# Performance work log

Hardware: AMD Instinct MI355X
Metric: run time of the kernel (lower is better)

## Reference

```python
import jax, jax.numpy as jnp
import numpy as np

N = 12000   # num_node
D = 128     # hiddenSize
HID = 256   # hidden_channels
B = 512     # batch
L = 20      # citing history length
F = 400     # title_vec + journal_vec
FF = 512    # transformer dim_feedforward
NH = 4      # heads
STDV = float(1.0 / np.sqrt(D))


def _unif(k, shape):
    return jax.random.uniform(k, shape, jnp.float32, -STDV, STDV)


def setup_inputs():
    key = jax.random.key(0)
    ks = jax.random.split(key, 40)
    inp = {}
    inp['embedding'] = _unif(ks[0], (N, D))
    inp['f1_w'] = _unif(ks[1], (D, F)); inp['f1_b'] = _unif(ks[2], (D,))
    # two GNN modules, each a 2-layer GCN (assumed structure)
    inp['gcn0_w1'] = _unif(ks[3], (D, HID)); inp['gcn0_b1'] = _unif(ks[4], (HID,))
    inp['gcn0_w2'] = _unif(ks[5], (HID, D)); inp['gcn0_b2'] = _unif(ks[6], (D,))
    inp['gcn1_w1'] = _unif(ks[7], (D, HID)); inp['gcn1_b1'] = _unif(ks[8], (HID,))
    inp['gcn1_w2'] = _unif(ks[9], (HID, D)); inp['gcn1_b2'] = _unif(ks[10], (D,))
    # transformer encoder layer (post-norm, relu), reset_parameters makes ALL weights uniform
    inp['in_proj_w'] = _unif(ks[11], (3 * D, D)); inp['in_proj_b'] = _unif(ks[12], (3 * D,))
    inp['out_proj_w'] = _unif(ks[13], (D, D)); inp['out_proj_b'] = _unif(ks[14], (D,))
    inp['ln1_s'] = _unif(ks[15], (D,)); inp['ln1_b'] = _unif(ks[16], (D,))
    inp['ff1_w'] = _unif(ks[17], (FF, D)); inp['ff1_b'] = _unif(ks[18], (FF,))
    inp['ff2_w'] = _unif(ks[19], (D, FF)); inp['ff2_b'] = _unif(ks[20], (D,))
    inp['ln2_s'] = _unif(ks[21], (D,)); inp['ln2_b'] = _unif(ks[22], (D,))
    # forward inputs
    inp['adj_mat'] = jax.random.uniform(ks[23], (N, N), jnp.float32) * (2.0 / N)  # ~row-stochastic
    inp['node_feature'] = jax.random.normal(ks[24], (N, F), jnp.float32)
    inp['H_content'] = jax.random.normal(ks[25], (B, 10), jnp.float32)  # unused in forward
    inp['citing'] = jax.random.randint(ks[26], (B,), 0, N)
    inp['h_items'] = jax.random.randint(ks[27], (B,), 0, N)  # unused in forward
    inp['u_seqs'] = jax.random.randint(ks[28], (B, L), 0, N)
    inp['u_seqs_num'] = jax.random.randint(ks[29], (B,), 1, L)  # unused in forward
    return inp


def _layer_norm(x, s, b):
    m = x.mean(-1, keepdims=True)
    v = ((x - m) ** 2).mean(-1, keepdims=True)
    return (x - m) * jax.lax.rsqrt(v + 1e-5) * s + b


def reference(embedding, f1_w, f1_b,
              gcn0_w1, gcn0_b1, gcn0_w2, gcn0_b2,
              gcn1_w1, gcn1_b1, gcn1_w2, gcn1_b2,
              in_proj_w, in_proj_b, out_proj_w, out_proj_b,
              ln1_s, ln1_b, ff1_w, ff1_b, ff2_w, ff2_b, ln2_s, ln2_b,
              adj_mat, node_feature, H_content,
              citing, h_items, u_seqs, u_seqs_num):
    # embedding gate
    nf = node_feature @ f1_w.T + f1_b          # [N, D]
    x = embedding * nf                          # [N, D]
    # GCN stack: each GNN = relu((A x) W1 + b1) -> (A h) W2 + b2
    for (w1, b1, w2, b2) in ((gcn0_w1, gcn0_b1, gcn0_w2, gcn0_b2),
                             (gcn1_w1, gcn1_b1, gcn1_w2, gcn1_b2)):
        h = jax.nn.relu((adj_mat @ x) @ w1 + b1)
        x = (adj_mat @ h) @ w2 + b2
    item = x                                    # [N, D]
    seq = item[u_seqs]                          # [B, L, D]
    # torch TransformerEncoderLayer with batch_first=False: dim0 (B) is the
    # sequence axis, dim1 (L) is the batch axis (faithful to original code).
    qkv = seq @ in_proj_w.T + in_proj_b         # [B, L, 3D]
    q, k, v = jnp.split(qkv, 3, axis=-1)
    dh = D // NH
    q = q.reshape(B, L, NH, dh) * (1.0 / np.sqrt(dh))
    k = k.reshape(B, L, NH, dh)
    v = v.reshape(B, L, NH, dh)
    att = jax.nn.softmax(jnp.einsum('snhd,tnhd->nhst', q, k), axis=-1)  # attn over seq axis s,t=B
    o = jnp.einsum('nhst,tnhd->snhd', att, v).reshape(B, L, D)
    o = o @ out_proj_w.T + out_proj_b
    x1 = _layer_norm(seq + o, ln1_s, ln1_b)
    ff = jax.nn.relu(x1 @ ff1_w.T + ff1_b) @ ff2_w.T + ff2_b
    x2 = _layer_norm(x1 + ff, ln2_s, ln2_b)
    citing_vec = x2.mean(axis=1)                # mean over dim=1 (L), [B, D]
    citing_feats = nf[citing]                   # [B, D]
    citing_paper = jnp.concatenate([citing_vec, citing_feats], axis=1)  # [B, 2D]
    cited_paper = jnp.concatenate([item, nf], axis=1)                   # [N, 2D]
    scores = citing_paper @ cited_paper.T       # [B, N]
    return scores
```

## Files before the change

### kernel.cpp

```cpp
#include <hip/hip_runtime.h>
#include <hip/hip_bf16.h>

typedef __hip_bfloat16 bf;
typedef __attribute__((ext_vector_type(4))) float f32x4;
typedef __attribute__((ext_vector_type(8))) __bf16 bf16x8;
typedef __attribute__((ext_vector_type(8))) short short8;

#define NN 12000
#define DD 128
#define HIDC 256
#define BBATCH 512
#define LSEQ 20
#define FFEAT 400
#define FFDIM 512

__device__ __forceinline__ float b2f(bf v) { return __bfloat162float(v); }
__device__ __forceinline__ bf f2b(float v) { return __float2bfloat16(v); }
__device__ __forceinline__ float us2f(unsigned short u) {
    return __uint_as_float(((unsigned int)u) << 16);
}
__device__ __forceinline__ unsigned short f2us(float f) {
    bf h = __float2bfloat16(f);
    return __builtin_bit_cast(unsigned short, h);
}

template<bool F32>
__device__ __forceinline__ short8 ld8(const void* p, long long idx) {
    if (F32) {
        const float* fp = (const float*)p + idx;
        f32x4 u0 = *(const f32x4*)fp;
        f32x4 u1 = *(const f32x4*)(fp + 4);
        short8 s;
        s[0] = (short)f2us(u0[0]); s[1] = (short)f2us(u0[1]);
        s[2] = (short)f2us(u0[2]); s[3] = (short)f2us(u0[3]);
        s[4] = (short)f2us(u1[0]); s[5] = (short)f2us(u1[1]);
        s[6] = (short)f2us(u1[2]); s[7] = (short)f2us(u1[3]);
        return s;
    } else {
        return *(const short8*)((const bf*)p + idx);
    }
}

template<bool F32>
__device__ __forceinline__ bf ldelem(const void* p, long long idx) {
    if (F32) return f2b(((const float*)p)[idx]);
    return ((const bf*)p)[idx];
}

template<bool A_F32, bool B_F32, bool HAS_BIAS, bool RELU, bool OUT_F32, bool SIDE_A>
__global__ __launch_bounds__(256) void gemm128(
    const void* __restrict__ A, int lda, long long sA1, long long sA2,
    const void* __restrict__ Bm, int ldb, long long sB1, long long sB2,
    const float* __restrict__ bias,
    void* __restrict__ Cv, int ldc, long long sC1, long long sC2,
    int M, int N, int K, int tilesN, int zdiv, float alpha,
    bf* __restrict__ sideA)
{
    __shared__ bf As[128][40];
    __shared__ bf Bs[128][40];
    const int tid = threadIdx.x;
    const int z = blockIdx.y;
    const int zq = z / zdiv, zr = z - zq * zdiv;
    const char* Ap = (const char*)A;
    const char* Bp = (const char*)Bm;
    const long long offA = (long long)zq * sA1 + (long long)zr * sA2;
    const long long offB = (long long)zq * sB1 + (long long)zr * sB2;
    const long long offC = (long long)zq * sC1 + (long long)zr * sC2;
    const int tm = blockIdx.x / tilesN, tn = blockIdx.x - tm * tilesN;
    int m0 = tm * 128; if (m0 > M - 128) m0 = M - 128;
    const int n0 = tn * 128;
    const int lane = tid & 63;
    const int wv = tid >> 6;
    const int wr = (wv >> 1) * 64, wc = (wv & 1) * 64;
    const int fr = lane & 15;
    const int kq = (lane >> 4) * 8;
    const int sr = tid >> 2, scol = (tid & 3) * 8;
    f32x4 acc[4][4] = {};

    for (int k0 = 0; k0 < K; k0 += 32) {
        if (k0 + 32 <= K) {
            const long long ia0 = offA + (long long)(m0 + sr) * lda + k0 + scol;
            const long long ia1 = offA + (long long)(m0 + sr + 64) * lda + k0 + scol;
            short8 va0 = ld8<A_F32>(Ap, ia0);
            short8 va1 = ld8<A_F32>(Ap, ia1);
            short8 vb0 = {0,0,0,0,0,0,0,0}, vb1 = {0,0,0,0,0,0,0,0};
            if (n0 + sr < N)      vb0 = ld8<B_F32>(Bp, offB + (long long)(n0 + sr) * ldb + k0 + scol);
            if (n0 + sr + 64 < N) vb1 = ld8<B_F32>(Bp, offB + (long long)(n0 + sr + 64) * ldb + k0 + scol);
            if (SIDE_A) {
                *(short8*)&sideA[ia0] = va0;
                *(short8*)&sideA[ia1] = va1;
            }
            *(short8*)&As[sr][scol] = va0;
            *(short8*)&As[sr + 64][scol] = va1;
            *(short8*)&Bs[sr][scol] = vb0;
            *(short8*)&Bs[sr + 64][scol] = vb1;
        } else {
            bf zv = f2b(0.f);
            for (int i = tid; i < 128 * 32; i += 256) {
                int r = i >> 5, c = i & 31, gk = k0 + c;
                As[r][c] = (gk < K) ? ldelem<A_F32>(Ap, offA + (long long)(m0 + r) * lda + gk) : zv;
                Bs[r][c] = (gk < K && n0 + r < N) ? ldelem<B_F32>(Bp, offB + (long long)(n0 + r) * ldb + gk) : zv;
            }
        }
        __syncthreads();
        bf16x8 af[4], bfg[4];
        #pragma unroll
        for (int i = 0; i < 4; i++) af[i]  = *(const bf16x8*)&As[wr + i * 16 + fr][kq];
        #pragma unroll
        for (int i = 0; i < 4; i++) bfg[i] = *(const bf16x8*)&Bs[wc + i * 16 + fr][kq];
        #pragma unroll
        for (int mi = 0; mi < 4; mi++)
            #pragma unroll
            for (int ni = 0; ni < 4; ni++)
                acc[mi][ni] = __builtin_amdgcn_mfma_f32_16x16x32_bf16(
                    af[mi], bfg[ni], acc[mi][ni], 0, 0, 0);
        __syncthreads();
    }

    const int cr0 = (lane >> 4) * 4;
    const int cc = lane & 15;
    #pragma unroll
    for (int mi = 0; mi < 4; mi++) {
        #pragma unroll
        for (int ni = 0; ni < 4; ni++) {
            int col = n0 + wc + ni * 16 + cc;
            if (col >= N) continue;
            float bv = 0.f;
            if (HAS_BIAS) bv = bias[col];
            #pragma unroll
            for (int j = 0; j < 4; j++) {
                int row = m0 + wr + mi * 16 + cr0 + j;
                float v = acc[mi][ni][j] * alpha + bv;
                if (RELU) v = fmaxf(v, 0.f);
                if (OUT_F32) ((float*)Cv)[offC + (long long)row * ldc + col] = v;
                else ((bf*)Cv)[offC + (long long)row * ldc + col] = f2b(v);
            }
        }
    }
}

template<bool IN_F32>
__global__ __launch_bounds__(256) void transpose_k(
    const void* __restrict__ in, int ldin, long long sI1, long long sI2, int zdiv,
    const float* __restrict__ mulp, int ldmul,
    bf* __restrict__ outp, int ldout, long long sOut,
    int R, int C)
{
    __shared__ bf t[32][33];
    const int z = blockIdx.z;
    const int zq = z / zdiv, zr = z - zq * zdiv;
    const long long offI = (long long)zq * sI1 + (long long)zr * sI2;
    bf* op = outp + (long long)z * sOut;
    int r0 = blockIdx.x * 32, c0 = blockIdx.y * 32;
    int tx = threadIdx.x, ty = threadIdx.y;
    #pragma unroll
    for (int i = 0; i < 4; i++) {
        int r = r0 + ty + i * 8, c = c0 + tx;
        bf v = f2b(0.f);
        if (r < R && c < C) {
            v = ldelem<IN_F32>(in, offI + (long long)r * ldin + c);
            if (mulp) v = f2b(b2f(v) * mulp[(long long)r * ldmul + c]);
        }
        t[ty + i * 8][tx] = v;
    }
    __syncthreads();
    #pragma unroll
    for (int i = 0; i < 4; i++) {
        int c = c0 + ty + i * 8, r = r0 + tx;
        if (c < C && r < R) op[(long long)c * ldout + r] = t[tx][ty + i * 8];
    }
}

__global__ __launch_bounds__(256) void reduceK(
    const float* __restrict__ part, const float* __restrict__ bias,
    bf* __restrict__ outp, int total, int nz, long long zs)
{
    int i = blockIdx.x * 256 + threadIdx.x;
    if (i >= total) return;
    float s = 0.f;
    for (int zz = 0; zz < nz; zz++) s += part[(long long)zz * zs + i];
    if (bias) s += bias[i & 127];
    outp[i] = f2b(s);
}

__global__ __launch_bounds__(256) void gather_rows(
    const bf* __restrict__ src, const int* __restrict__ idx,
    bf* __restrict__ dst, int nrows)
{
    int t = blockIdx.x * 256 + threadIdx.x;
    int row = t >> 4, p = t & 15;
    if (row >= nrows) return;
    long long srow = idx[row];
    *(short8*)&dst[(long long)row * 128 + p * 8] =
        *(const short8*)&src[srow * 128 + p * 8];
}

__global__ __launch_bounds__(256) void softmax512(bf* __restrict__ S, int nrows)
{
    int gid = blockIdx.x * 256 + threadIdx.x;
    int wid = gid >> 6, lane = gid & 63;
    if (wid >= nrows) return;
    bf* row = S + (long long)wid * 512;
    short8 raw = *(const short8*)&row[lane * 8];
    float v[8];
    float mx = -3.0e38f;
    #pragma unroll
    for (int j = 0; j < 8; j++) {
        v[j] = us2f((unsigned short)raw[j]);
        mx = fmaxf(mx, v[j]);
    }
    #pragma unroll
    for (int off = 32; off; off >>= 1) mx = fmaxf(mx, __shfl_xor(mx, off, 64));
    float sum = 0.f;
    #pragma unroll
    for (int j = 0; j < 8; j++) { v[j] = __expf(v[j] - mx); sum += v[j]; }
    #pragma unroll
    for (int off = 32; off; off >>= 1) sum += __shfl_xor(sum, off, 64);
    float inv = 1.f / sum;
    short8 o;
    #pragma unroll
    for (int j = 0; j < 8; j++) o[j] = (short)f2us(v[j] * inv);
    *(short8*)&row[lane * 8] = o;
}

__global__ __launch_bounds__(256) void ln_rows(
    const bf* __restrict__ a, const bf* __restrict__ bres,
    const float* __restrict__ sc, const float* __restrict__ bi,
    bf* __restrict__ outp, int nrows)
{
    int gid = blockIdx.x * 256 + threadIdx.x;
    int wid = gid >> 6, lane = gid & 63;
    if (wid >= nrows) return;
    long long base = (long long)wid * 128;
    int i0 = lane * 2, i1 = lane * 2 + 1;
    float x0 = b2f(a[base + i0]) + b2f(bres[base + i0]);
    float x1 = b2f(a[base + i1]) + b2f(bres[base + i1]);
    float s = x0 + x1;
    #pragma unroll
    for (int off = 32; off; off >>= 1) s += __shfl_xor(s, off, 64);
    float mean = s * (1.f / 128.f);
    float d0 = x0 - mean, d1 = x1 - mean;
    float vv = d0 * d0 + d1 * d1;
    #pragma unroll
    for (int off = 32; off; off >>= 1) vv += __shfl_xor(vv, off, 64);
    float inv = rsqrtf(vv * (1.f / 128.f) + 1e-5f);
    outp[base + i0] = f2b(d0 * inv * sc[i0] + bi[i0]);
    outp[base + i1] = f2b(d1 * inv * sc[i1] + bi[i1]);
}

__global__ __launch_bounds__(256) void build_citing(
    const bf* __restrict__ x2, const bf* __restrict__ nf,
    const int* __restrict__ citing, bf* __restrict__ cp)
{
    int i = blockIdx.x * 256 + threadIdx.x;
    if (i >= BBATCH * 256) return;
    int b = i >> 8, d = i & 255;
    float v;
    if (d < 128) {
        float s = 0.f;
        for (int l = 0; l < LSEQ; l++)
            s += b2f(x2[((long long)b * LSEQ + l) * 128 + d]);
        v = s * (1.f / (float)LSEQ);
    } else {
        v = b2f(nf[(long long)citing[b] * 128 + (d - 128)]);
    }
    cp[i] = f2b(v);
}

__global__ __launch_bounds__(256) void build_cited(
    const bf* __restrict__ item, const bf* __restrict__ nf, bf* __restrict__ outp)
{
    int i = blockIdx.x * 256 + threadIdx.x;
    if (i >= NN * 256) return;
    int r = i >> 8, d = i & 255;
    outp[i] = (d < 128) ? item[(long long)r * 128 + d]
                        : nf[(long long)r * 128 + (d - 128)];
}

extern "C" void kernel_launch(void* const* d_in, const int* in_sizes, int n_in,
                              void* d_out, int out_size, void* d_ws, size_t ws_size,
                              hipStream_t stream)
{
    const float* emb  = (const float*)d_in[0];
    const float* f1w  = (const float*)d_in[1];
    const float* f1b  = (const float*)d_in[2];
    const float* g0w1 = (const float*)d_in[3];  const float* g0b1 = (const float*)d_in[4];
    const float* g0w2 = (const float*)d_in[5];  const float* g0b2 = (const float*)d_in[6];
    const float* g1w1 = (const float*)d_in[7];  const float* g1b1 = (const float*)d_in[8];
    const float* g1w2 = (const float*)d_in[9];  const float* g1b2 = (const float*)d_in[10];
    const float* ipw  = (const float*)d_in[11]; const float* ipb  = (const float*)d_in[12];
    const float* opw  = (const float*)d_in[13]; const float* opb  = (const float*)d_in[14];
    const float* ln1s = (const float*)d_in[15]; const float* ln1b = (const float*)d_in[16];
    const float* ff1w = (const float*)d_in[17]; const float* ff1b = (const float*)d_in[18];
    const float* ff2w = (const float*)d_in[19]; const float* ff2b = (const float*)d_in[20];
    const float* ln2s = (const float*)d_in[21]; const float* ln2b = (const float*)d_in[22];
    const float* adj  = (const float*)d_in[23];
    const float* nfe  = (const float*)d_in[24];
    const int* citing = (const int*)d_in[26];
    const int* useqs  = (const int*)d_in[28];
    float* outp = (float*)d_out;

    size_t off = 0;
    auto carve = [&](size_t bytes) -> char* {
        char* p = (char*)d_ws + off;
        off += (bytes + 255) & ~(size_t)255;
        return p;
    };
    bf* adjb = (bf*)carve((size_t)NN * NN * 2);
    bf* nf   = (bf*)carve((size_t)NN * DD * 2);
    bf* bufP = (bf*)carve((size_t)NN * DD * 2);
    bf* bufQ = (bf*)carve((size_t)NN * DD * 2);
    bf* BT   = (bf*)carve((size_t)NN * DD * 2);
    bf* Hbuf = (bf*)carve((size_t)NN * HIDC * 2);
    float* part = (float*)carve((size_t)5 * NN * DD * 4);
    bf* seq  = (bf*)carve((size_t)10240 * DD * 2);
    bf* qkv  = (bf*)carve((size_t)10240 * 384 * 2);
    bf* Sb   = (bf*)carve((size_t)80 * 512 * 512 * 2);
    bf* w10T = (bf*)carve((size_t)DD * HIDC * 2);
    bf* w20T = (bf*)carve((size_t)DD * HIDC * 2);
    bf* w11T = (bf*)carve((size_t)DD * HIDC * 2);
    bf* w21T = (bf*)carve((size_t)DD * HIDC * 2);
    bf* x1ln = (bf*)Hbuf;
    bf* cp   = (bf*)((char*)Hbuf + (size_t)10240 * DD * 2);
    char* pr = (char*)part;
    bf* VT   = (bf*)pr; pr += (size_t)80 * 32 * 512 * 2;
    bf* o_   = (bf*)pr; pr += (size_t)10240 * DD * 2;
    bf* o2   = (bf*)pr; pr += (size_t)10240 * DD * 2;
    bf* ffh  = (bf*)pr; pr += (size_t)10240 * FFDIM * 2;
    bf* ff2o = (bf*)pr; pr += (size_t)10240 * DD * 2;
    bf* x2   = (bf*)pr; pr += (size_t)10240 * DD * 2;
    bf* cited= (bf*)pr; pr += (size_t)NN * 256 * 2;

    dim3 tb(256), tt(32, 8);
    const long long NM = (long long)NN * DD;

    transpose_k<true><<<dim3(4, 8, 1), tt, 0, stream>>>(g0w1, HIDC, 0, 0, 1, nullptr, 0, w10T, DD, 0, DD, HIDC);
    transpose_k<true><<<dim3(8, 4, 1), tt, 0, stream>>>(g0w2, DD, 0, 0, 1, nullptr, 0, w20T, HIDC, 0, HIDC, DD);
    transpose_k<true><<<dim3(4, 8, 1), tt, 0, stream>>>(g1w1, HIDC, 0, 0, 1, nullptr, 0, w11T, DD, 0, DD, HIDC);
    transpose_k<true><<<dim3(8, 4, 1), tt, 0, stream>>>(g1w2, DD, 0, 0, 1, nullptr, 0, w21T, HIDC, 0, HIDC, DD);

    gemm128<true, true, true, false, false, false><<<dim3(94, 1), tb, 0, stream>>>(
        nfe, FFEAT, 0, 0, f1w, FFEAT, 0, 0, f1b,
        nf, DD, 0, 0, NN, DD, FFEAT, 1, 1, 1.f, nullptr);
    transpose_k<false><<<dim3(375, 4, 1), tt, 0, stream>>>(nf, DD, 0, 0, 1, emb, DD, BT, NN, 0, NN, DD);

    const float* biases2[2] = { g0b2, g1b2 };
    const float* biases1[2] = { g0b1, g1b1 };
    const bf* w1T[2] = { w10T, w11T };
    const bf* w2T[2] = { w20T, w21T };
    bf* xout[2] = { bufP, bufQ };

    for (int g = 0; g < 2; g++) {
        if (g == 0) {
            gemm128<true, false, false, false, true, true><<<dim3(94, 5), tb, 0, stream>>>(
                adj, NN, 2400, 0, BT, NN, 2400, 0, nullptr,
                part, DD, NM, 0, NN, DD, 2400, 1, 1, 1.f, adjb);
        } else {
            gemm128<false, false, false, false, true, false><<<dim3(94, 5), tb, 0, stream>>>(
                adjb, NN, 2400, 0, BT, NN, 2400, 0, nullptr,
                part, DD, NM, 0, NN, DD, 2400, 1, 1, 1.f, nullptr);
        }
        bf* tbuf = (g == 0) ? bufP : bufQ;
        reduceK<<<dim3((NM + 255) / 256), tb, 0, stream>>>(part, nullptr, tbuf, (int)NM, 5, NM);
        gemm128<false, false, true, true, false, false><<<dim3(188, 1), tb, 0, stream>>>(
            tbuf, DD, 0, 0, w1T[g], DD, 0, 0, biases1[g],
            Hbuf, HIDC, 0, 0, NN, HIDC, DD, 2, 1, 1.f, nullptr);
        bf* t2buf = (g == 0) ? bufQ : bufP;
        gemm128<false, false, false, false, false, false><<<dim3(94, 1), tb, 0, stream>>>(
            Hbuf, HIDC, 0, 0, w2T[g], HIDC, 0, 0, nullptr,
            t2buf, DD, 0, 0, NN, DD, HIDC, 1, 1, 1.f, nullptr);
        transpose_k<false><<<dim3(375, 4, 1), tt, 0, stream>>>(t2buf, DD, 0, 0, 1, nullptr, 0, BT, NN, 0, NN, DD);
        gemm128<false, false, false, false, true, false><<<dim3(94, 5), tb, 0, stream>>>(
            adjb, NN, 2400, 0, BT, NN, 2400, 0, nullptr,
            part, DD, NM, 0, NN, DD, 2400, 1, 1, 1.f, nullptr);
        reduceK<<<dim3((NM + 255) / 256), tb, 0, stream>>>(part, biases2[g], xout[g], (int)NM, 5, NM);
        if (g == 0) {
            transpose_k<false><<<dim3(375, 4, 1), tt, 0, stream>>>(bufP, DD, 0, 0, 1, nullptr, 0, BT, NN, 0, NN, DD);
        }
    }
    bf* item = bufQ;

    gather_rows<<<dim3(640), tb, 0, stream>>>(item, useqs, seq, 10240);
    gemm128<false, true, true, false, false, false><<<dim3(240, 1), tb, 0, stream>>>(
        seq, DD, 0, 0, ipw, DD, 0, 0, ipb,
        qkv, 384, 0, 0, 10240, 384, DD, 3, 1, 1.f, nullptr);
    transpose_k<false><<<dim3(16, 1, 80), tt, 0, stream>>>(
        qkv + 256, 7680, 384, 32, 4, nullptr, 0, VT, 512, 16384, 512, 32);
    gemm128<false, false, false, false, false, false><<<dim3(16, 80), tb, 0, stream>>>(
        qkv, 7680, 384, 32, qkv + 128, 7680, 384, 32, nullptr,
        Sb, 512, (long long)4 * 262144, 262144, 512, 512, 32, 4, 4, 0.17677669529663687f, nullptr);
    softmax512<<<dim3(10240), tb, 0, stream>>>(Sb, 80 * 512);
    gemm128<false, false, false, false, false, false><<<dim3(4, 80), tb, 0, stream>>>(
        Sb, 512, (long long)4 * 262144, 262144, VT, 512, (long long)4 * 16384, 16384, nullptr,
        o_, 2560, 128, 32, 512, 32, 512, 1, 4, 1.f, nullptr);
    gemm128<false, true, true, false, false, false><<<dim3(80, 1), tb, 0, stream>>>(
        o_, DD, 0, 0, opw, DD, 0, 0, opb,
        o2, DD, 0, 0, 10240, DD, DD, 1, 1, 1.f, nullptr);
    ln_rows<<<dim3(2560), tb, 0, stream>>>(seq, o2, ln1s, ln1b, x1ln, 10240);
    gemm128<false, true, true, true, false, false><<<dim3(320, 1), tb, 0, stream>>>(
        x1ln, DD, 0, 0, ff1w, DD, 0, 0, ff1b,
        ffh, FFDIM, 0, 0, 10240, FFDIM, DD, 4, 1, 1.f, nullptr);
    gemm128<false, true, true, false, false, false><<<dim3(80, 1), tb, 0, stream>>>(
        ffh, FFDIM, 0, 0, ff2w, FFDIM, 0, 0, ff2b,
        ff2o, DD, 0, 0, 10240, DD, FFDIM, 1, 1, 1.f, nullptr);
    ln_rows<<<dim3(2560), tb, 0, stream>>>(x1ln, ff2o, ln2s, ln2b, x2, 10240);
    build_citing<<<dim3(512), tb, 0, stream>>>(x2, nf, citing, cp);
    build_cited<<<dim3(12000), tb, 0, stream>>>(item, nf, cited);
    gemm128<false, false, false, false, true, false><<<dim3(376, 1), tb, 0, stream>>>(
        cp, 256, 0, 0, cited, 256, 0, 0, nullptr,
        outp, NN, 0, 0, BBATCH, NN, 256, 94, 1, 1.f, nullptr);
}
```

Baseline: 812.1 us.

## Add register-only MFMA kernel for bf16 adjacency split-K GEMMs

```diff
diff --git a/kernel.cpp b/kernel.cpp
--- a/kernel.cpp
+++ b/kernel.cpp
@@ -13,6 +13,9 @@
 #define LSEQ 20
 #define FFEAT 400
 #define FFDIM 512
+#define AZ 5
+#define AKS (NN / AZ)
+#define ANT (AKS / 32)
 
 __device__ __forceinline__ float b2f(bf v) { return __bfloat162float(v); }
 __device__ __forceinline__ bf f2b(float v) { return __float2bfloat16(v); }
@@ -45,6 +48,89 @@
 __device__ __forceinline__ bf ldelem(const void* p, long long idx) {
     if (F32) return f2b(((const float*)p)[idx]);
     return ((const bf*)p)[idx];
+}
+
+__global__ __launch_bounds__(256) void adj_gemm5(
+    const bf* __restrict__ A,
+    const bf* __restrict__ Bt,
+    float* __restrict__ part)
+{
+    const int tid = threadIdx.x;
+    const int lane = tid & 63;
+    const int w = tid >> 6;
+    const int z = blockIdx.y;
+    const long long k0 = (long long)z * AKS;
+    int strip = blockIdx.x * 4 + w;
+    if (strip > NN / 32 - 1) strip = NN / 32 - 1;
+    const int m0 = strip * 32;
+
+    const int fr = lane & 15;
+    const int kq = (lane >> 4) * 8;
+
+    const bf* pa0 = A + (long long)(m0 + fr) * NN + k0 + kq;
+    const bf* pa1 = A + (long long)(m0 + 16 + fr) * NN + k0 + kq;
+    const bf* pb  = Bt + (long long)fr * NN + k0 + kq;
+
+    f32x4 acc[2][8] = {};
+    bf16x8 aE[2], bE[8], aO[2], bO[8];
+
+    auto loadE = [&](int t) {
+        const long long o = (long long)t * 32;
+        aE[0] = *(const bf16x8*)(pa0 + o);
+        aE[1] = *(const bf16x8*)(pa1 + o);
+        #pragma unroll
+        for (int c = 0; c < 8; c++)
+            bE[c] = *(const bf16x8*)(pb + (long long)c * (16 * NN) + o);
+    };
+    auto loadO = [&](int t) {
+        const long long o = (long long)t * 32;
+        aO[0] = *(const bf16x8*)(pa0 + o);
+        aO[1] = *(const bf16x8*)(pa1 + o);
+        #pragma unroll
+        for (int c = 0; c < 8; c++)
+            bO[c] = *(const bf16x8*)(pb + (long long)c * (16 * NN) + o);
+    };
+    auto mfmaE = [&]() {
+        #pragma unroll
+        for (int mi = 0; mi < 2; mi++)
+            #pragma unroll
+            for (int c = 0; c < 8; c++)
+                acc[mi][c] = __builtin_amdgcn_mfma_f32_16x16x32_bf16(
+                    aE[mi], bE[c], acc[mi][c], 0, 0, 0);
+    };
+    auto mfmaO = [&]() {
+        #pragma unroll
+        for (int mi = 0; mi < 2; mi++)
+            #pragma unroll
+            for (int c = 0; c < 8; c++)
+                acc[mi][c] = __builtin_amdgcn_mfma_f32_16x16x32_bf16(
+                    aO[mi], bO[c], acc[mi][c], 0, 0, 0);
+    };
+
+    loadE(0);
+    #pragma unroll 1
+    for (int ks = 0; ks < ANT - 1; ks += 2) {
+        loadO(ks + 1);
+        mfmaE();
+        if (ks + 2 < ANT) loadE(ks + 2);
+        mfmaO();
+    }
+    mfmaE();
+
+    float* C = part + (long long)z * ((long long)NN * 128);
+    const int cr0 = (lane >> 4) * 4;
+    const int cc = lane & 15;
+    #pragma unroll
+    for (int mi = 0; mi < 2; mi++) {
+        #pragma unroll
+        for (int c = 0; c < 8; c++) {
+            #pragma unroll
+            for (int j = 0; j < 4; j++) {
+                int row = m0 + mi * 16 + cr0 + j;
+                C[(long long)row * 128 + c * 16 + cc] = acc[mi][c][j];
+            }
+        }
+    }
 }
 
 template<bool A_F32, bool B_F32, bool HAS_BIAS, bool RELU, bool OUT_F32, bool SIDE_A>
@@ -312,7 +398,7 @@
     bf* bufQ = (bf*)carve((size_t)NN * DD * 2);
     bf* BT   = (bf*)carve((size_t)NN * DD * 2);
     bf* Hbuf = (bf*)carve((size_t)NN * HIDC * 2);
-    float* part = (float*)carve((size_t)5 * NN * DD * 4);
+    float* part = (float*)carve((size_t)AZ * NN * DD * 4);
     bf* seq  = (bf*)carve((size_t)10240 * DD * 2);
     bf* qkv  = (bf*)carve((size_t)10240 * 384 * 2);
     bf* Sb   = (bf*)carve((size_t)80 * 512 * 512 * 2);
@@ -352,16 +438,14 @@
 
     for (int g = 0; g < 2; g++) {
         if (g == 0) {
-            gemm128<true, false, false, false, true, true><<<dim3(94, 5), tb, 0, stream>>>(
-                adj, NN, 2400, 0, BT, NN, 2400, 0, nullptr,
-                part, DD, NM, 0, NN, DD, 2400, 1, 1, 1.f, adjb);
+            gemm128<true, false, false, false, true, true><<<dim3(94, AZ), tb, 0, stream>>>(
+                adj, NN, AKS, 0, BT, NN, AKS, 0, nullptr,
+                part, DD, NM, 0, NN, DD, AKS, 1, 1, 1.f, adjb);
         } else {
-            gemm128<false, false, false, false, true, false><<<dim3(94, 5), tb, 0, stream>>>(
-                adjb, NN, 2400, 0, BT, NN, 2400, 0, nullptr,
-                part, DD, NM, 0, NN, DD, 2400, 1, 1, 1.f, nullptr);
+            adj_gemm5<<<dim3(94, AZ), tb, 0, stream>>>(adjb, BT, part);
         }
         bf* tbuf = (g == 0) ? bufP : bufQ;
-        reduceK<<<dim3((NM + 255) / 256), tb, 0, stream>>>(part, nullptr, tbuf, (int)NM, 5, NM);
+        reduceK<<<dim3((NM + 255) / 256), tb, 0, stream>>>(part, nullptr, tbuf, (int)NM, AZ, NM);
         gemm128<false, false, true, true, false, false><<<dim3(188, 1), tb, 0, stream>>>(
             tbuf, DD, 0, 0, w1T[g], DD, 0, 0, biases1[g],
             Hbuf, HIDC, 0, 0, NN, HIDC, DD, 2, 1, 1.f, nullptr);
@@ -370,10 +454,8 @@
             Hbuf, HIDC, 0, 0, w2T[g], HIDC, 0, 0, nullptr,
             t2buf, DD, 0, 0, NN, DD, HIDC, 1, 1, 1.f, nullptr);
         transpose_k<false><<<dim3(375, 4, 1), tt, 0, stream>>>(t2buf, DD, 0, 0, 1, nullptr, 0, BT, NN, 0, NN, DD);
-        gemm128<false, false, false, false, true, false><<<dim3(94, 5), tb, 0, stream>>>(
-            adjb, NN, 2400, 0, BT, NN, 2400, 0, nullptr,
-            part, DD, NM, 0, NN, DD, 2400, 1, 1, 1.f, nullptr);
-        reduceK<<<dim3((NM + 255) / 256), tb, 0, stream>>>(part, biases2[g], xout[g], (int)NM, 5, NM);
+        adj_gemm5<<<dim3(94, AZ), tb, 0, stream>>>(adjb, BT, part);
+        reduceK<<<dim3((NM + 255) / 256), tb, 0, stream>>>(part, biases2[g], xout[g], (int)NM, AZ, NM);
         if (g == 0) {
             transpose_k<false><<<dim3(375, 4, 1), tt, 0, stream>>>(bufP, DD, 0, 0, 1, nullptr, 0, BT, NN, 0, NN, DD);
         }
```

Measured after the change: 1.019 ms. +25.5%, slower.
